# Optimization experiments

Hardware: AMD Instinct MI355X
Metric: run time of the kernel (lower is better)

The kernel has to match this reference:

```python
import jax, jax.numpy as jnp
import numpy as np

H = 512   # embedding_dim (forced by Attention(512,512))
F = 21    # n_features
T = 28    # output_length

def _cell(x, h, c, Wih, Whh, b):
    # PyTorch LSTMCell math, gate order i,f,g,o
    g = x @ Wih.T + h @ Whh.T + b
    i, f, gg, o = jnp.split(g, 4, axis=-1)
    c2 = jax.nn.sigmoid(f) * c + jax.nn.sigmoid(i) * jnp.tanh(gg)
    h2 = jax.nn.sigmoid(o) * jnp.tanh(c2)
    return h2, c2

def _lstm3(inp, h, c, Wih0, Wih1, Wih2, Whh, bih, bhh):
    # 3-layer LSTM, single time step. h,c: [3,1,H]
    Wihs = (Wih0, Wih1, Wih2)
    hs, cs = [], []
    x = inp
    for l in range(3):
        hl, cl = _cell(x, h[l], c[l], Wihs[l], Whh[l], bih[l] + bhh[l])
        hs.append(hl); cs.append(cl)
        x = hl
    return x, jnp.stack(hs), jnp.stack(cs)

def setup_inputs() -> dict:
    key = jax.random.key(0)
    ks = jax.random.split(key, 20)
    s = 0.05
    f32 = jnp.float32
    return {
        "x": jax.random.normal(ks[0], (1, F), f32),
        "prev_y": jax.random.normal(ks[1], (1, F), f32),
        "enc_Wih0": jax.random.normal(ks[2], (4*H, F), f32) * s,
        "enc_Wih1": jax.random.normal(ks[3], (4*H, H), f32) * s,
        "enc_Wih2": jax.random.normal(ks[4], (4*H, H), f32) * s,
        "enc_Whh": jax.random.normal(ks[5], (3, 4*H, H), f32) * s,
        "enc_bih": jax.random.normal(ks[6], (3, 4*H), f32) * s,
        "enc_bhh": jax.random.normal(ks[7], (3, 4*H), f32) * s,
        "attn_W": jax.random.normal(ks[8], (H, 2*H), f32) * s,
        "attn_b": jax.random.normal(ks[9], (H,), f32) * s,
        "v_W": jax.random.normal(ks[10], (1, H), f32) * s,
        "dec_Wih0": jax.random.normal(ks[11], (4*H, H+F), f32) * s,
        "dec_Wih1": jax.random.normal(ks[12], (4*H, H), f32) * s,
        "dec_Wih2": jax.random.normal(ks[13], (4*H, H), f32) * s,
        "dec_Whh": jax.random.normal(ks[14], (3, 4*H, H), f32) * s,
        "dec_bih": jax.random.normal(ks[15], (3, 4*H), f32) * s,
        "dec_bhh": jax.random.normal(ks[16], (3, 4*H), f32) * s,
        "out_W": jax.random.normal(ks[17], (F, 2*H), f32) * s,
        "out_b": jax.random.normal(ks[18], (F,), f32) * s,
    }

def reference(x, prev_y, enc_Wih0, enc_Wih1, enc_Wih2, enc_Whh, enc_bih, enc_bhh,
              attn_W, attn_b, v_W, dec_Wih0, dec_Wih1, dec_Wih2, dec_Whh, dec_bih, dec_bhh,
              out_W, out_b):
    z = jnp.zeros((3, 1, H), x.dtype)
    # Encoder: single time step over feature-as-sequence input [1, F]
    enc_out, h, c = _lstm3(x, z, z, enc_Wih0, enc_Wih1, enc_Wih2, enc_Whh, enc_bih, enc_bhh)
    # enc_out: [1, H]; src_len == 1

    def step(carry, _):
        prev_out, h, c = carry
        # Bahdanau attention (src_len = 1)
        cat = jnp.concatenate([h[2], enc_out], axis=-1)          # [1, 2H]
        energy = jnp.tanh(cat @ attn_W.T + attn_b)               # [1, H]
        score = energy @ v_W.T                                    # [1, 1]
        a = jax.nn.softmax(score, axis=1)                         # [1, 1] (== 1)
        weighted = a * enc_out                                    # [1, H]
        rnn_in = jnp.concatenate([prev_out, weighted], axis=-1)  # [1, H+F]
        out, h2, c2 = _lstm3(rnn_in, h, c, dec_Wih0, dec_Wih1, dec_Wih2, dec_Whh, dec_bih, dec_bhh)
        y = jnp.concatenate([out, weighted], axis=-1) @ out_W.T + out_b  # [1, F]
        return (y, h2, c2), y

    _, ys = jax.lax.scan(step, (prev_y, h, c), None, length=T)
    return ys  # [T, 1, F]
```

## Files before the change

kernel.cpp:

```cpp
#include <hip/hip_runtime.h>
#include <cstddef>

constexpr int H  = 512;
constexpr int F  = 21;
constexpr int T  = 28;
constexpr int PB = 128;
constexpr int NB = PB + 1;
constexpr int NT = 256;
constexpr int NW = NT / 64;

#define SCOPE_AGENT __HIP_MEMORY_SCOPE_AGENT

__device__ __align__(16) unsigned long long g_hp[2][3][H];
__device__ __align__(16) unsigned long long g_hy[T][H];
__device__ unsigned g_epoch;

struct P {
  const float *x, *py, *eW0, *eW1, *eW2, *ebih, *ebhh;
  const float *dW0, *dW1, *dW2, *dWhh, *dbih, *dbhh, *outW, *outb;
  float* out;
};

__device__ __forceinline__ float sigm(float v)  { return 1.0f / (1.0f + __expf(-v)); }
__device__ __forceinline__ float tanh_f(float v){ return 1.0f - 2.0f / (__expf(2.0f * v) + 1.0f); }

__device__ __forceinline__ float4 wredsum4(float4 v) {
#pragma unroll
  for (int off = 32; off > 0; off >>= 1) {
    v.x += __shfl_xor(v.x, off, 64);
    v.y += __shfl_xor(v.y, off, 64);
    v.z += __shfl_xor(v.z, off, 64);
    v.w += __shfl_xor(v.w, off, 64);
  }
  return v;
}
__device__ __forceinline__ float wredsum1(float v) {
#pragma unroll
  for (int off = 32; off > 0; off >>= 1) v += __shfl_xor(v, off, 64);
  return v;
}

__device__ __forceinline__ void pput(unsigned long long* slot, float v, unsigned tag) {
  union { float f; unsigned u; } c; c.f = v;
  unsigned long long pk = ((unsigned long long)tag << 32) | (unsigned long long)c.u;
  (void)__hip_atomic_exchange(slot, pk, __ATOMIC_RELAXED, SCOPE_AGENT);
}

typedef unsigned int u32x4 __attribute__((ext_vector_type(4)));
__device__ __forceinline__ u32x4 tld16(const unsigned long long* q) {
  u32x4 r;
  asm volatile("global_load_dwordx4 %0, %1, off sc1\n\t"
               "s_waitcnt vmcnt(0)"
               : "=v"(r) : "v"(q) : "memory");
  return r;
}

__device__ __forceinline__ void stagev(const unsigned long long* __restrict__ A,
                                       unsigned wa, float* __restrict__ dst) {
  const int i = threadIdx.x;
  u32x4 v = tld16(A + 2 * i);
  int guard = 0;
  while ((v.y != wa || v.w != wa) && ++guard < (1 << 20)) v = tld16(A + 2 * i);
  *(float2*)(dst + 2 * i) = make_float2(__uint_as_float(v.x), __uint_as_float(v.z));
  __syncthreads();
}

struct W8 { float4 a[4]; float4 b[4]; };

__device__ __forceinline__ W8 ldw_g(const float* __restrict__ W, int r, int lane) {
  W8 o;
#pragma unroll
  for (int g = 0; g < 4; ++g) {
    const float* q = W + (size_t)(g * H + r) * H + lane * 8;
    o.a[g] = *(const float4*)q;
    o.b[g] = *(const float4*)(q + 4);
  }
  return o;
}
__device__ __forceinline__ void fma8(const W8& wt, const float4& x0, const float4& x1,
                                     float s[4]) {
#pragma unroll
  for (int g = 0; g < 4; ++g) {
    s[g] += wt.a[g].x * x0.x + wt.a[g].y * x0.y + wt.a[g].z * x0.z + wt.a[g].w * x0.w
          + wt.b[g].x * x1.x + wt.b[g].y * x1.y + wt.b[g].z * x1.z + wt.b[g].w * x1.w;
  }
}

__device__ __forceinline__ float cellup(const float4& v, const float b[4], float& c) {
  float cn = sigm(v.y + b[1]) * c + sigm(v.x + b[0]) * tanh_f(v.z + b[2]);
  c = cn;
  return sigm(v.w + b[3]) * tanh_f(cn);
}

__device__ __forceinline__ void write_y_frag(const P& p, int trow, int w, int lane,
                                             const float4& h0, const float4& h1,
                                             const float* sYe) {
  for (int j = w; j < F; j += NW) {
    const float* q = p.outW + (size_t)j * (2 * H) + lane * 8;
    float4 w0 = *(const float4*)q;
    float4 w1 = *(const float4*)(q + 4);
    float s = w0.x * h0.x + w0.y * h0.y + w0.z * h0.z + w0.w * h0.w
            + w1.x * h1.x + w1.y * h1.y + w1.z * h1.z + w1.w * h1.w;
    s = wredsum1(s);
    if (lane == 0) p.out[trow * F + j] = s + sYe[j];
  }
}

__global__ __launch_bounds__(NT, 1)
void k_flow(P p) {
  const int lane = threadIdx.x & 63;
  const int w    = threadIdx.x >> 6;
  const unsigned ep =
      __hip_atomic_load(&g_epoch, __ATOMIC_RELAXED, SCOPE_AGENT) << 6;

  __shared__ float sBuf[2][H];
  __shared__ float senc[H];
  __shared__ float sYe[F + 3];

  if (blockIdx.x == PB) {
    stagev(g_hp[1][2], ep + 1u, senc);
    {
      float4 e0 = *(const float4*)(senc + lane * 8);
      float4 e1 = *(const float4*)(senc + lane * 8 + 4);
      for (int j = w; j < F; j += NW) {
        const float* q = p.outW + (size_t)j * (2 * H) + H + lane * 8;
        float4 w0 = *(const float4*)q;
        float4 w1 = *(const float4*)(q + 4);
        float s = w0.x * e0.x + w0.y * e0.y + w0.z * e0.z + w0.w * e0.w
                + w1.x * e1.x + w1.y * e1.y + w1.z * e1.z + w1.w * e1.w;
        s = wredsum1(s);
        if (lane == 0) sYe[j] = s + p.outb[j];
      }
      __syncthreads();
    }
    for (int t = 0; t < T; ++t) {
      float* xb = sBuf[t & 1];
      stagev(g_hy[t], ep + (unsigned)(t + 2), xb);
      float4 h20 = *(const float4*)(xb + lane * 8);
      float4 h21 = *(const float4*)(xb + lane * 8 + 4);
      write_y_frag(p, t, w, lane, h20, h21, sYe);
    }
    if (threadIdx.x == 0)
      __hip_atomic_fetch_add(&g_epoch, 1u, __ATOMIC_RELAXED, SCOPE_AGENT);
  } else {
    const int r = blockIdx.x * NW + w;

    float c0 = 0.f, c1 = 0.f, c2 = 0.f;
    float b00[4], b0p[4], b1s[4], b2s[4];
    float sOld0[4] = {0, 0, 0, 0}, sOld1[4] = {0, 0, 0, 0}, sOld2[4] = {0, 0, 0, 0};
    int bi = 0;

    {
      float s0 = 0.f, s1 = 0.f, s2 = 0.f, s3 = 0.f;
      if (lane < F) {
        const float xv = p.x[lane];
        s0 = p.eW0[(size_t)(0 * H + r) * F + lane] * xv;
        s1 = p.eW0[(size_t)(1 * H + r) * F + lane] * xv;
        s2 = p.eW0[(size_t)(2 * H + r) * F + lane] * xv;
        s3 = p.eW0[(size_t)(3 * H + r) * F + lane] * xv;
      }
      float4 v = wredsum4(make_float4(s0, s1, s2, s3));
      if (lane == 0) {
        const float* bi_ = p.ebih + r;
        const float* bh_ = p.ebhh + r;
        float cn = sigm(v.x + bi_[0] + bh_[0]) * tanh_f(v.z + bi_[2 * H] + bh_[2 * H]);
        c0 = cn;
        pput(&g_hp[1][0][r], sigm(v.w + bi_[3 * H] + bh_[3 * H]) * tanh_f(cn), ep + 1u);
      }
    }

    W8 wM;
    {
#pragma unroll
      for (int g = 0; g < 4; ++g) {
        wM.a[g] = make_float4(0.f, 0.f, 0.f, 0.f);
        wM.b[g] = make_float4(0.f, 0.f, 0.f, 0.f);
      }
      for (int f = 0; f < F; ++f) {
        const float* q = p.outW + (size_t)f * (2 * H) + lane * 8;
        const float4 oa  = *(const float4*)q;
        const float4 obv = *(const float4*)(q + 4);
#pragma unroll
        for (int g = 0; g < 4; ++g) {
          const float wf = p.dW0[(size_t)(g * H + r) * (H + F) + f];
          wM.a[g].x += wf * oa.x;  wM.a[g].y += wf * oa.y;
          wM.a[g].z += wf * oa.z;  wM.a[g].w += wf * oa.w;
          wM.b[g].x += wf * obv.x; wM.b[g].y += wf * obv.y;
          wM.b[g].z += wf * obv.z; wM.b[g].w += wf * obv.w;
        }
      }
    }
    W8 wD1 = ldw_g(p.dW1, r, lane);
    W8 wD2 = ldw_g(p.dW2, r, lane);

#pragma unroll
    for (int g = 0; g < 4; ++g) {
      b1s[g] = p.dbih[4 * H + g * H + r] + p.dbhh[4 * H + g * H + r];
      b2s[g] = p.dbih[8 * H + g * H + r] + p.dbhh[8 * H + g * H + r];
    }

    {
      W8 wt = ldw_g(p.eW1, r, lane);
      stagev(g_hp[1][0], ep + 1u, sBuf[0]);
      float4 a0 = *(const float4*)(sBuf[0] + lane * 8);
      float4 a1 = *(const float4*)(sBuf[0] + lane * 8 + 4);
      float s[4] = {0.f, 0.f, 0.f, 0.f};
      fma8(wt, a0, a1, s);
      float4 v = wredsum4(make_float4(s[0], s[1], s[2], s[3]));
      if (lane == 0) {
        const float* bi_ = p.ebih + 4 * H + r;
        const float* bh_ = p.ebhh + 4 * H + r;
        float cn = sigm(v.x + bi_[0] + bh_[0]) * tanh_f(v.z + bi_[2 * H] + bh_[2 * H]);
        c1 = cn;
        pput(&g_hp[1][1][r], sigm(v.w + bi_[3 * H] + bh_[3 * H]) * tanh_f(cn), ep + 1u);
      }
    }

    {
      W8 wt  = ldw_g(p.eW2, r, lane);
      W8 wh1 = ldw_g(p.dWhh + (size_t)4 * H * H, r, lane);
      stagev(g_hp[1][1], ep + 1u, sBuf[1]);
      float4 a0 = *(const float4*)(sBuf[1] + lane * 8);
      float4 a1 = *(const float4*)(sBuf[1] + lane * 8 + 4);
      float s[4] = {0.f, 0.f, 0.f, 0.f};
      fma8(wt, a0, a1, s);
      float4 v = wredsum4(make_float4(s[0], s[1], s[2], s[3]));
      if (lane == 0) {
        const float* bi_ = p.ebih + 8 * H + r;
        const float* bh_ = p.ebhh + 8 * H + r;
        float cn = sigm(v.x + bi_[0] + bh_[0]) * tanh_f(v.z + bi_[2 * H] + bh_[2 * H]);
        c2 = cn;
        pput(&g_hp[1][2][r], sigm(v.w + bi_[3 * H] + bh_[3 * H]) * tanh_f(cn), ep + 1u);
      }
      fma8(wh1, a0, a1, sOld1);
    }

    W8 wh00;
    {
      W8 wh2 = ldw_g(p.dWhh + (size_t)8 * H * H, r, lane);
      stagev(g_hp[1][2], ep + 1u, senc);
      float4 e0 = *(const float4*)(senc + lane * 8);
      float4 e1 = *(const float4*)(senc + lane * 8 + 4);
      for (int j = w; j < F; j += NW) {
        const float* q = p.outW + (size_t)j * (2 * H) + H + lane * 8;
        float4 w0 = *(const float4*)q;
        float4 w1 = *(const float4*)(q + 4);
        float s = w0.x * e0.x + w0.y * e0.y + w0.z * e0.z + w0.w * e0.w
                + w1.x * e1.x + w1.y * e1.y + w1.z * e1.z + w1.w * e1.w;
        s = wredsum1(s);
        if (lane == 0) sYe[j] = s + p.outb[j];
      }
      {
        float sg[4];
#pragma unroll
        for (int g = 0; g < 4; ++g) {
          const float* q = p.dW0 + (size_t)(g * H + r) * (H + F) + F + lane * 8;
          sg[g] = q[0] * e0.x + q[1] * e0.y + q[2] * e0.z + q[3] * e0.w
                + q[4] * e1.x + q[5] * e1.y + q[6] * e1.z + q[7] * e1.w;
        }
        float4 v = wredsum4(make_float4(sg[0], sg[1], sg[2], sg[3]));
        if (lane == 0) {
          b0p[0] = v.x + p.dbih[0 * H + r] + p.dbhh[0 * H + r];
          b0p[1] = v.y + p.dbih[1 * H + r] + p.dbhh[1 * H + r];
          b0p[2] = v.z + p.dbih[2 * H + r] + p.dbhh[2 * H + r];
          b0p[3] = v.w + p.dbih[3 * H + r] + p.dbhh[3 * H + r];
        }
      }
      wh00 = ldw_g(p.dWhh, r, lane);
      {
        float f0 = 0.f, f1 = 0.f, f2 = 0.f, f3 = 0.f;
        if (lane < F) {
          const float yv = p.py[lane];
          f0 = p.dW0[(size_t)(0 * H + r) * (H + F) + lane] * yv;
          f1 = p.dW0[(size_t)(1 * H + r) * (H + F) + lane] * yv;
          f2 = p.dW0[(size_t)(2 * H + r) * (H + F) + lane] * yv;
          f3 = p.dW0[(size_t)(3 * H + r) * (H + F) + lane] * yv;
        }
        float4 v = wredsum4(make_float4(f0, f1, f2, f3));
        if (lane == 0) {
          b00[0] = b0p[0] + v.x; b00[1] = b0p[1] + v.y;
          b00[2] = b0p[2] + v.z; b00[3] = b0p[3] + v.w;
        }
      }
      __syncthreads();
      {
        float f0 = 0.f, f1 = 0.f, f2 = 0.f, f3 = 0.f;
        if (lane < F) {
          const float yv = sYe[lane];
          f0 = p.dW0[(size_t)(0 * H + r) * (H + F) + lane] * yv;
          f1 = p.dW0[(size_t)(1 * H + r) * (H + F) + lane] * yv;
          f2 = p.dW0[(size_t)(2 * H + r) * (H + F) + lane] * yv;
          f3 = p.dW0[(size_t)(3 * H + r) * (H + F) + lane] * yv;
        }
        float4 v = wredsum4(make_float4(f0, f1, f2, f3));
        if (lane == 0) {
          b0p[0] += v.x; b0p[1] += v.y; b0p[2] += v.z; b0p[3] += v.w;
        }
      }
      fma8(wh2, e0, e1, sOld2);
    }

    {
      float4 a0 = *(const float4*)(sBuf[0] + lane * 8);
      float4 a1 = *(const float4*)(sBuf[0] + lane * 8 + 4);
      float s[4] = {0.f, 0.f, 0.f, 0.f};
      fma8(wh00, a0, a1, s);
      float4 v = wredsum4(make_float4(s[0], s[1], s[2], s[3]));
      if (lane == 0) pput(&g_hp[0][0][r], cellup(v, b00, c0), ep + 2u);
    }
    __syncthreads();

    for (int t = 0; t < T; ++t) {
      const int pb = t & 1, ob = pb ^ 1;
      const unsigned wn = ep + (unsigned)(t + 2);
      const unsigned wo = wn - 1u;

      if (t >= 1) {
        stagev(g_hp[ob][2], wo, sBuf[bi]);
        W8 wh2 = ldw_g(p.dWhh + (size_t)8 * H * H, r, lane);
        float4 h20 = *(const float4*)(sBuf[bi] + lane * 8);
        float4 h21 = *(const float4*)(sBuf[bi] + lane * 8 + 4);
        float s[4] = {sOld0[0], sOld0[1], sOld0[2], sOld0[3]};
        fma8(wM, h20, h21, s);
        float4 v = wredsum4(make_float4(s[0], s[1], s[2], s[3]));
        if (lane == 0) pput(&g_hp[pb][0][r], cellup(v, b0p, c0), wn);
        sOld2[0] = sOld2[1] = sOld2[2] = sOld2[3] = 0.f;
        fma8(wh2, h20, h21, sOld2);
        bi ^= 1;
      }

      {
        stagev(g_hp[pb][0], wn, sBuf[bi]);
        W8 wh0 = ldw_g(p.dWhh, r, lane);
        float4 a0 = *(const float4*)(sBuf[bi] + lane * 8);
        float4 a1 = *(const float4*)(sBuf[bi] + lane * 8 + 4);
        float s[4] = {sOld1[0], sOld1[1], sOld1[2], sOld1[3]};
        fma8(wD1, a0, a1, s);
        float4 v = wredsum4(make_float4(s[0], s[1], s[2], s[3]));
        if (lane == 0) pput(&g_hp[pb][1][r], cellup(v, b1s, c1), wn);
        sOld0[0] = sOld0[1] = sOld0[2] = sOld0[3] = 0.f;
        fma8(wh0, a0, a1, sOld0);
        bi ^= 1;
      }
      {
        stagev(g_hp[pb][1], wn, sBuf[bi]);
        W8 wh1 = ldw_g(p.dWhh + (size_t)4 * H * H, r, lane);
        float4 a0 = *(const float4*)(sBuf[bi] + lane * 8);
        float4 a1 = *(const float4*)(sBuf[bi] + lane * 8 + 4);
        float s[4] = {sOld2[0], sOld2[1], sOld2[2], sOld2[3]};
        fma8(wD2, a0, a1, s);
        float4 v = wredsum4(make_float4(s[0], s[1], s[2], s[3]));
        if (lane == 0) {
          float hv = cellup(v, b2s, c2);
          pput(&g_hp[pb][2][r], hv, wn);
          pput(&g_hy[t][r], hv, wn);
        }
        sOld1[0] = sOld1[1] = sOld1[2] = sOld1[3] = 0.f;
        fma8(wh1, a0, a1, sOld1);
        bi ^= 1;
      }
    }
  }
}

extern "C" void kernel_launch(void* const* d_in, const int* in_sizes, int n_in,
                              void* d_out, int out_size, void* d_ws, size_t ws_size,
                              hipStream_t stream) {
  P p;
  p.x    = (const float*)d_in[0];
  p.py   = (const float*)d_in[1];
  p.eW0  = (const float*)d_in[2];
  p.eW1  = (const float*)d_in[3];
  p.eW2  = (const float*)d_in[4];
  p.ebih = (const float*)d_in[6];
  p.ebhh = (const float*)d_in[7];
  p.dW0  = (const float*)d_in[11];
  p.dW1  = (const float*)d_in[12];
  p.dW2  = (const float*)d_in[13];
  p.dWhh = (const float*)d_in[14];
  p.dbih = (const float*)d_in[15];
  p.dbhh = (const float*)d_in[16];
  p.outW = (const float*)d_in[17];
  p.outb = (const float*)d_in[18];
  p.out  = (float*)d_out;

  hipLaunchKernelGGL(k_flow, dim3(NB), dim3(NT), 0, stream, p);
}
```

Before: 333.8 us.

## Gate per-vector polling behind a global arrival counter per stage

Replaces the per-element tag-polling stage with a two-phase scheme. Thread 0 of each block bumps a per-stage global counter and spins on it until all producer blocks have arrived, and only then do the threads load the tagged vector, which should now rarely need re-polling. The encoder outputs move into dedicated buffers. The intent is to cut the heavy memory traffic of 256 threads per block repeatedly polling remote slots. The cost is an extra atomic plus a serial spin on one thread per stage, with two more block barriers.

```diff
diff --git a/kernel.cpp b/kernel.cpp
--- a/kernel.cpp
+++ b/kernel.cpp
@@ -11,8 +11,12 @@
 
 #define SCOPE_AGENT __HIP_MEMORY_SCOPE_AGENT
 
+__device__ __align__(16) unsigned long long g_eh0[H];
+__device__ __align__(16) unsigned long long g_eh1[H];
+__device__ __align__(16) unsigned long long g_enc[H];
 __device__ __align__(16) unsigned long long g_hp[2][3][H];
 __device__ __align__(16) unsigned long long g_hy[T][H];
+__device__ unsigned g_cnt[128];
 __device__ unsigned g_epoch;
 
 struct P {
@@ -54,13 +58,31 @@
                : "=v"(r) : "v"(q) : "memory");
   return r;
 }
-
-__device__ __forceinline__ void stagev(const unsigned long long* __restrict__ A,
-                                       unsigned wa, float* __restrict__ dst) {
+__device__ __forceinline__ unsigned cld(const unsigned* q) {
+  unsigned r;
+  asm volatile("global_load_dword %0, %1, off sc1\n\t"
+               "s_waitcnt vmcnt(0)"
+               : "=v"(r) : "v"(q) : "memory");
+  return r;
+}
+
+__device__ __forceinline__ void stageg(const unsigned long long* __restrict__ A,
+                                       unsigned tag, unsigned* __restrict__ cnt,
+                                       unsigned expect, bool contribute,
+                                       float* __restrict__ dst) {
+  __syncthreads();
+  if (threadIdx.x == 0) {
+    if (contribute)
+      (void)__hip_atomic_fetch_add(cnt, 1u, __ATOMIC_RELAXED, SCOPE_AGENT);
+    unsigned c = cld(cnt);
+    int g = 0;
+    while (c < expect && ++g < (1 << 22)) c = cld(cnt);
+  }
+  __syncthreads();
   const int i = threadIdx.x;
   u32x4 v = tld16(A + 2 * i);
-  int guard = 0;
-  while ((v.y != wa || v.w != wa) && ++guard < (1 << 20)) v = tld16(A + 2 * i);
+  int g2 = 0;
+  while ((v.y != tag || v.w != tag) && ++g2 < (1 << 20)) v = tld16(A + 2 * i);
   *(float2*)(dst + 2 * i) = make_float2(__uint_as_float(v.x), __uint_as_float(v.z));
   __syncthreads();
 }
@@ -110,15 +132,17 @@
 void k_flow(P p) {
   const int lane = threadIdx.x & 63;
   const int w    = threadIdx.x >> 6;
-  const unsigned ep =
-      __hip_atomic_load(&g_epoch, __ATOMIC_RELAXED, SCOPE_AGENT) << 6;
+  const unsigned ep_raw =
+      __hip_atomic_load(&g_epoch, __ATOMIC_RELAXED, SCOPE_AGENT);
+  const unsigned tg     = ep_raw << 6;
+  const unsigned expect = ep_raw * (unsigned)PB + (unsigned)PB;
 
   __shared__ float sBuf[2][H];
   __shared__ float senc[H];
   __shared__ float sYe[F + 3];
 
   if (blockIdx.x == PB) {
-    stagev(g_hp[1][2], ep + 1u, senc);
+    stageg(g_enc, tg + 1u, &g_cnt[2], expect, false, senc);
     {
       float4 e0 = *(const float4*)(senc + lane * 8);
       float4 e1 = *(const float4*)(senc + lane * 8 + 4);
@@ -135,7 +159,8 @@
     }
     for (int t = 0; t < T; ++t) {
       float* xb = sBuf[t & 1];
-      stagev(g_hy[t], ep + (unsigned)(t + 2), xb);
+      stageg(g_hy[t], tg + (unsigned)(t + 2), &g_cnt[3 + 3 * t + 2], expect,
+             false, xb);
       float4 h20 = *(const float4*)(xb + lane * 8);
       float4 h21 = *(const float4*)(xb + lane * 8 + 4);
       write_y_frag(p, t, w, lane, h20, h21, sYe);
@@ -165,7 +190,7 @@
         const float* bh_ = p.ebhh + r;
         float cn = sigm(v.x + bi_[0] + bh_[0]) * tanh_f(v.z + bi_[2 * H] + bh_[2 * H]);
         c0 = cn;
-        pput(&g_hp[1][0][r], sigm(v.w + bi_[3 * H] + bh_[3 * H]) * tanh_f(cn), ep + 1u);
+        pput(&g_eh0[r], sigm(v.w + bi_[3 * H] + bh_[3 * H]) * tanh_f(cn), tg + 1u);
       }
     }
 
@@ -201,7 +226,7 @@
 
     {
       W8 wt = ldw_g(p.eW1, r, lane);
-      stagev(g_hp[1][0], ep + 1u, sBuf[0]);
+      stageg(g_eh0, tg + 1u, &g_cnt[0], expect, true, sBuf[0]);
       float4 a0 = *(const float4*)(sBuf[0] + lane * 8);
       float4 a1 = *(const float4*)(sBuf[0] + lane * 8 + 4);
       float s[4] = {0.f, 0.f, 0.f, 0.f};
@@ -212,14 +237,14 @@
         const float* bh_ = p.ebhh + 4 * H + r;
         float cn = sigm(v.x + bi_[0] + bh_[0]) * tanh_f(v.z + bi_[2 * H] + bh_[2 * H]);
         c1 = cn;
-        pput(&g_hp[1][1][r], sigm(v.w + bi_[3 * H] + bh_[3 * H]) * tanh_f(cn), ep + 1u);
+        pput(&g_eh1[r], sigm(v.w + bi_[3 * H] + bh_[3 * H]) * tanh_f(cn), tg + 1u);
       }
     }
 
     {
       W8 wt  = ldw_g(p.eW2, r, lane);
       W8 wh1 = ldw_g(p.dWhh + (size_t)4 * H * H, r, lane);
-      stagev(g_hp[1][1], ep + 1u, sBuf[1]);
+      stageg(g_eh1, tg + 1u, &g_cnt[1], expect, true, sBuf[1]);
       float4 a0 = *(const float4*)(sBuf[1] + lane * 8);
       float4 a1 = *(const float4*)(sBuf[1] + lane * 8 + 4);
       float s[4] = {0.f, 0.f, 0.f, 0.f};
@@ -230,7 +255,7 @@
         const float* bh_ = p.ebhh + 8 * H + r;
         float cn = sigm(v.x + bi_[0] + bh_[0]) * tanh_f(v.z + bi_[2 * H] + bh_[2 * H]);
         c2 = cn;
-        pput(&g_hp[1][2][r], sigm(v.w + bi_[3 * H] + bh_[3 * H]) * tanh_f(cn), ep + 1u);
+        pput(&g_enc[r], sigm(v.w + bi_[3 * H] + bh_[3 * H]) * tanh_f(cn), tg + 1u);
       }
       fma8(wh1, a0, a1, sOld1);
     }
@@ -238,7 +263,7 @@
     W8 wh00;
     {
       W8 wh2 = ldw_g(p.dWhh + (size_t)8 * H * H, r, lane);
-      stagev(g_hp[1][2], ep + 1u, senc);
+      stageg(g_enc, tg + 1u, &g_cnt[2], expect, true, senc);
       float4 e0 = *(const float4*)(senc + lane * 8);
       float4 e1 = *(const float4*)(senc + lane * 8 + 4);
       for (int j = w; j < F; j += NW) {
@@ -306,17 +331,16 @@
       float s[4] = {0.f, 0.f, 0.f, 0.f};
       fma8(wh00, a0, a1, s);
       float4 v = wredsum4(make_float4(s[0], s[1], s[2], s[3]));
-      if (lane == 0) pput(&g_hp[0][0][r], cellup(v, b00, c0), ep + 2u);
-    }
-    __syncthreads();
+      if (lane == 0) pput(&g_hp[0][0][r], cellup(v, b00, c0), tg + 2u);
+    }
 
     for (int t = 0; t < T; ++t) {
       const int pb = t & 1, ob = pb ^ 1;
-      const unsigned wn = ep + (unsigned)(t + 2);
+      const unsigned wn = tg + (unsigned)(t + 2);
       const unsigned wo = wn - 1u;
 
       if (t >= 1) {
-        stagev(g_hp[ob][2], wo, sBuf[bi]);
+        stageg(g_hp[ob][2], wo, &g_cnt[3 * t + 2], expect, true, sBuf[bi]);
         W8 wh2 = ldw_g(p.dWhh + (size_t)8 * H * H, r, lane);
         float4 h20 = *(const float4*)(sBuf[bi] + lane * 8);
         float4 h21 = *(const float4*)(sBuf[bi] + lane * 8 + 4);
@@ -330,7 +354,7 @@
       }
 
       {
-        stagev(g_hp[pb][0], wn, sBuf[bi]);
+        stageg(g_hp[pb][0], wn, &g_cnt[3 + 3 * t + 0], expect, true, sBuf[bi]);
         W8 wh0 = ldw_g(p.dWhh, r, lane);
         float4 a0 = *(const float4*)(sBuf[bi] + lane * 8);
         float4 a1 = *(const float4*)(sBuf[bi] + lane * 8 + 4);
@@ -343,7 +367,7 @@
         bi ^= 1;
       }
       {
-        stagev(g_hp[pb][1], wn, sBuf[bi]);
+        stageg(g_hp[pb][1], wn, &g_cnt[3 + 3 * t + 1], expect, true, sBuf[bi]);
         W8 wh1 = ldw_g(p.dWhh + (size_t)4 * H * H, r, lane);
         float4 a0 = *(const float4*)(sBuf[bi] + lane * 8);
         float4 a1 = *(const float4*)(sBuf[bi] + lane * 8 + 4);
@@ -360,6 +384,11 @@
         bi ^= 1;
       }
     }
+
+    __syncthreads();
+    if (threadIdx.x == 0)
+      (void)__hip_atomic_fetch_add(&g_cnt[3 + 3 * (T - 1) + 2], 1u,
+                                   __ATOMIC_RELAXED, SCOPE_AGENT);
   }
 }
 
```

After: 472.6 us. 1.42x slower.

## Use atomic 8-byte polling loads, separate encoder buffers, and hoist weight loads

Applied to the files above, without the earlier changes.

Replaces the inline-asm 16-byte sc1 polling load with two relaxed agent-scope atomic 8-byte loads per thread, issued as a pair before the value is checked. Encoder hidden states move to dedicated global buffers so they no longer alias the decoder ping-pong buffers. Each recurrent weight load (ldw_g) now sits before the spin-wait, so its memory latency overlaps the wait for the previous layer. The intent is shorter critical-path latency per step, at the cost of more load instructions and higher register pressure from weights held during the spin.

```diff
diff --git a/kernel.cpp b/kernel.cpp
--- a/kernel.cpp
+++ b/kernel.cpp
@@ -11,6 +11,9 @@
 
 #define SCOPE_AGENT __HIP_MEMORY_SCOPE_AGENT
 
+__device__ __align__(16) unsigned long long g_eh0[H];
+__device__ __align__(16) unsigned long long g_eh1[H];
+__device__ __align__(16) unsigned long long g_enc[H];
 __device__ __align__(16) unsigned long long g_hp[2][3][H];
 __device__ __align__(16) unsigned long long g_hy[T][H];
 __device__ unsigned g_epoch;
@@ -45,23 +48,25 @@
   unsigned long long pk = ((unsigned long long)tag << 32) | (unsigned long long)c.u;
   (void)__hip_atomic_exchange(slot, pk, __ATOMIC_RELAXED, SCOPE_AGENT);
 }
-
-typedef unsigned int u32x4 __attribute__((ext_vector_type(4)));
-__device__ __forceinline__ u32x4 tld16(const unsigned long long* q) {
-  u32x4 r;
-  asm volatile("global_load_dwordx4 %0, %1, off sc1\n\t"
-               "s_waitcnt vmcnt(0)"
-               : "=v"(r) : "v"(q) : "memory");
-  return r;
+__device__ __forceinline__ unsigned long long tld(const unsigned long long* q) {
+  return __hip_atomic_load(q, __ATOMIC_RELAXED, SCOPE_AGENT);
+}
+__device__ __forceinline__ float fbits(unsigned long long v) {
+  union { unsigned u; float f; } c; c.u = (unsigned)v; return c.f;
 }
 
 __device__ __forceinline__ void stagev(const unsigned long long* __restrict__ A,
                                        unsigned wa, float* __restrict__ dst) {
   const int i = threadIdx.x;
-  u32x4 v = tld16(A + 2 * i);
+  unsigned long long v0 = tld(A + i), v1 = tld(A + i + NT);
+  unsigned long long w0 = tld(A + i), w1 = tld(A + i + NT);
   int guard = 0;
-  while ((v.y != wa || v.w != wa) && ++guard < (1 << 20)) v = tld16(A + 2 * i);
-  *(float2*)(dst + 2 * i) = make_float2(__uint_as_float(v.x), __uint_as_float(v.z));
+  while ((((unsigned)(v0 >> 32)) != wa || ((unsigned)(v1 >> 32)) != wa) &&
+         ++guard < (1 << 20)) {
+    v0 = w0; v1 = w1;
+    w0 = tld(A + i); w1 = tld(A + i + NT);
+  }
+  dst[i] = fbits(v0); dst[i + NT] = fbits(v1);
   __syncthreads();
 }
 
@@ -110,7 +115,7 @@
 void k_flow(P p) {
   const int lane = threadIdx.x & 63;
   const int w    = threadIdx.x >> 6;
-  const unsigned ep =
+  const unsigned tg =
       __hip_atomic_load(&g_epoch, __ATOMIC_RELAXED, SCOPE_AGENT) << 6;
 
   __shared__ float sBuf[2][H];
@@ -118,7 +123,7 @@
   __shared__ float sYe[F + 3];
 
   if (blockIdx.x == PB) {
-    stagev(g_hp[1][2], ep + 1u, senc);
+    stagev(g_enc, tg + 1u, senc);
     {
       float4 e0 = *(const float4*)(senc + lane * 8);
       float4 e1 = *(const float4*)(senc + lane * 8 + 4);
@@ -135,7 +140,7 @@
     }
     for (int t = 0; t < T; ++t) {
       float* xb = sBuf[t & 1];
-      stagev(g_hy[t], ep + (unsigned)(t + 2), xb);
+      stagev(g_hy[t], tg + (unsigned)(t + 2), xb);
       float4 h20 = *(const float4*)(xb + lane * 8);
       float4 h21 = *(const float4*)(xb + lane * 8 + 4);
       write_y_frag(p, t, w, lane, h20, h21, sYe);
@@ -165,7 +170,7 @@
         const float* bh_ = p.ebhh + r;
         float cn = sigm(v.x + bi_[0] + bh_[0]) * tanh_f(v.z + bi_[2 * H] + bh_[2 * H]);
         c0 = cn;
-        pput(&g_hp[1][0][r], sigm(v.w + bi_[3 * H] + bh_[3 * H]) * tanh_f(cn), ep + 1u);
+        pput(&g_eh0[r], sigm(v.w + bi_[3 * H] + bh_[3 * H]) * tanh_f(cn), tg + 1u);
       }
     }
 
@@ -201,7 +206,7 @@
 
     {
       W8 wt = ldw_g(p.eW1, r, lane);
-      stagev(g_hp[1][0], ep + 1u, sBuf[0]);
+      stagev(g_eh0, tg + 1u, sBuf[0]);
       float4 a0 = *(const float4*)(sBuf[0] + lane * 8);
       float4 a1 = *(const float4*)(sBuf[0] + lane * 8 + 4);
       float s[4] = {0.f, 0.f, 0.f, 0.f};
@@ -212,14 +217,14 @@
         const float* bh_ = p.ebhh + 4 * H + r;
         float cn = sigm(v.x + bi_[0] + bh_[0]) * tanh_f(v.z + bi_[2 * H] + bh_[2 * H]);
         c1 = cn;
-        pput(&g_hp[1][1][r], sigm(v.w + bi_[3 * H] + bh_[3 * H]) * tanh_f(cn), ep + 1u);
+        pput(&g_eh1[r], sigm(v.w + bi_[3 * H] + bh_[3 * H]) * tanh_f(cn), tg + 1u);
       }
     }
 
     {
       W8 wt  = ldw_g(p.eW2, r, lane);
       W8 wh1 = ldw_g(p.dWhh + (size_t)4 * H * H, r, lane);
-      stagev(g_hp[1][1], ep + 1u, sBuf[1]);
+      stagev(g_eh1, tg + 1u, sBuf[1]);
       float4 a0 = *(const float4*)(sBuf[1] + lane * 8);
       float4 a1 = *(const float4*)(sBuf[1] + lane * 8 + 4);
       float s[4] = {0.f, 0.f, 0.f, 0.f};
@@ -230,7 +235,7 @@
         const float* bh_ = p.ebhh + 8 * H + r;
         float cn = sigm(v.x + bi_[0] + bh_[0]) * tanh_f(v.z + bi_[2 * H] + bh_[2 * H]);
         c2 = cn;
-        pput(&g_hp[1][2][r], sigm(v.w + bi_[3 * H] + bh_[3 * H]) * tanh_f(cn), ep + 1u);
+        pput(&g_enc[r], sigm(v.w + bi_[3 * H] + bh_[3 * H]) * tanh_f(cn), tg + 1u);
       }
       fma8(wh1, a0, a1, sOld1);
     }
@@ -238,7 +243,7 @@
     W8 wh00;
     {
       W8 wh2 = ldw_g(p.dWhh + (size_t)8 * H * H, r, lane);
-      stagev(g_hp[1][2], ep + 1u, senc);
+      stagev(g_enc, tg + 1u, senc);
       float4 e0 = *(const float4*)(senc + lane * 8);
       float4 e1 = *(const float4*)(senc + lane * 8 + 4);
       for (int j = w; j < F; j += NW) {
@@ -306,18 +311,18 @@
       float s[4] = {0.f, 0.f, 0.f, 0.f};
       fma8(wh00, a0, a1, s);
       float4 v = wredsum4(make_float4(s[0], s[1], s[2], s[3]));
-      if (lane == 0) pput(&g_hp[0][0][r], cellup(v, b00, c0), ep + 2u);
+      if (lane == 0) pput(&g_hp[0][0][r], cellup(v, b00, c0), tg + 2u);
     }
     __syncthreads();
 
     for (int t = 0; t < T; ++t) {
       const int pb = t & 1, ob = pb ^ 1;
-      const unsigned wn = ep + (unsigned)(t + 2);
+      const unsigned wn = tg + (unsigned)(t + 2);
       const unsigned wo = wn - 1u;
 
       if (t >= 1) {
+        W8 wh2 = ldw_g(p.dWhh + (size_t)8 * H * H, r, lane);
         stagev(g_hp[ob][2], wo, sBuf[bi]);
-        W8 wh2 = ldw_g(p.dWhh + (size_t)8 * H * H, r, lane);
         float4 h20 = *(const float4*)(sBuf[bi] + lane * 8);
         float4 h21 = *(const float4*)(sBuf[bi] + lane * 8 + 4);
         float s[4] = {sOld0[0], sOld0[1], sOld0[2], sOld0[3]};
@@ -330,8 +335,8 @@
       }
 
       {
+        W8 wh0 = ldw_g(p.dWhh, r, lane);
         stagev(g_hp[pb][0], wn, sBuf[bi]);
-        W8 wh0 = ldw_g(p.dWhh, r, lane);
         float4 a0 = *(const float4*)(sBuf[bi] + lane * 8);
         float4 a1 = *(const float4*)(sBuf[bi] + lane * 8 + 4);
         float s[4] = {sOld1[0], sOld1[1], sOld1[2], sOld1[3]};
@@ -343,8 +348,8 @@
         bi ^= 1;
       }
       {
+        W8 wh1 = ldw_g(p.dWhh + (size_t)4 * H * H, r, lane);
         stagev(g_hp[pb][1], wn, sBuf[bi]);
-        W8 wh1 = ldw_g(p.dWhh + (size_t)4 * H * H, r, lane);
         float4 a0 = *(const float4*)(sBuf[bi] + lane * 8);
         float4 a1 = *(const float4*)(sBuf[bi] + lane * 8 + 4);
         float s[4] = {sOld2[0], sOld2[1], sOld2[2], sOld2[3]};
```

Measured after the change: 366.9 us. +9.9%, slower.
